# Optimization experiments

Measured on AMD Instinct MI355X. Metric: run time of the kernel, lower is better.

Reference implementation:

```python
import jax, jax.numpy as jnp
import numpy as np

N_ATOMS = 512
B = 14            # orbitals per atom (basis block size)
F = 128           # node feature dim
FE = 128          # edge feature dim
HID = 256
P = N_ATOMS * (N_ATOMS - 1) // 2


def setup_inputs() -> dict:
    key = jax.random.key(0)
    ks = jax.random.split(key, 12)
    s = 0.02  # small init scale for MLP weights
    pi, pj = jnp.triu_indices(N_ATOMS, k=1)
    return {
        "nodes_feature": jax.random.normal(ks[0], (N_ATOMS, F), jnp.float32),
        "edges_feature": jax.random.normal(ks[1], (N_ATOMS, N_ATOMS, FE), jnp.float32),
        "atom_blocks": jax.random.normal(ks[2], (N_ATOMS, B, B), jnp.float32),
        "overlap_pair": jax.random.normal(ks[3], (P, B, B), jnp.float32),
        "W1": jax.random.normal(ks[4], (F + FE, HID), jnp.float32) * s,
        "b1": jnp.zeros((HID,), jnp.float32),
        "W2": jax.random.normal(ks[5], (HID, B * B), jnp.float32) * s,
        "b2": jnp.zeros((B * B,), jnp.float32),
        "Wo1": jax.random.normal(ks[6], (2 * F + FE, HID), jnp.float32) * s,
        "bo1": jnp.zeros((HID,), jnp.float32),
        "Wo2": jax.random.normal(ks[7], (HID, B * B), jnp.float32) * s,
        "bo2": jnp.zeros((B * B,), jnp.float32),
        "pair_i": pi.astype(jnp.int32),
        "pair_j": pj.astype(jnp.int32),
    }


def reference(nodes_feature, edges_feature, atom_blocks, overlap_pair,
              W1, b1, W2, b2, Wo1, bo1, Wo2, bo2, pair_i, pair_j):
    n = nodes_feature.shape[0]
    ar = jnp.arange(n)

    # ---- diagonal blocks: MLP(node_i, edge_ii) -> BxB correction of atom block
    e_ii = edges_feature[ar, ar]                          # [N, FE]
    x = jnp.concatenate([nodes_feature, e_ii], axis=-1)   # [N, F+FE]
    h = jax.nn.silu(x @ W1 + b1)
    m = (h @ W2 + b2).reshape(n, B, B)
    diag_blocks = atom_blocks + m                         # [N, B, B]

    # ---- off-diagonal blocks: MLP(node_i, node_j, edge_ij) -> BxB correction
    ni = nodes_feature[pair_i]                            # [P, F]
    nj = nodes_feature[pair_j]                            # [P, F]
    eij = edges_feature[pair_i, pair_j]                   # [P, FE]
    xo = jnp.concatenate([ni, nj, eij], axis=-1)          # [P, 2F+FE]
    ho = jax.nn.silu(xo @ Wo1 + bo1)
    mo = (ho @ Wo2 + bo2).reshape(-1, B, B)
    off_blocks = overlap_pair + mo                        # [P, B, B]

    # ---- scatter blocks into dense Hamiltonian [N*B, N*B]
    Hm = jnp.zeros((n, B, n, B), dtype=nodes_feature.dtype)
    Hm = Hm.at[ar, :, ar, :].set(diag_blocks)
    Hm = Hm.at[pair_i, :, pair_j, :].set(off_blocks)
    Hm = Hm.at[pair_j, :, pair_i, :].set(jnp.transpose(off_blocks, (0, 2, 1)))
    return Hm.reshape(n * B, n * B)
```

## Files before the change

kernel.cpp:

```cpp
#include <hip/hip_runtime.h>
#include <stdint.h>

typedef unsigned short u16;
typedef unsigned int u32;
typedef __bf16 bf16x8 __attribute__((ext_vector_type(8)));
typedef float f32x4 __attribute__((ext_vector_type(4)));

#define N_ATOMS 512
#define BDIM 14
#define BB 196
#define FDIM 128
#define HROW 7168
#define NPAIR 130816
#define ROWS 64
#define NPBLK (NPAIR / ROWS)
#define NBLK  (NPBLK + N_ATOMS / ROWS)
#define HALFU (ROWS * BB / 2)

#define OFF_W1F   0
#define OFF_W2F   65536
#define OFF_WO1F  118784
#define OFF_WO2F  217088
#define WS_ELEMS  270336

__device__ __forceinline__ float b2f(u16 u) {
    union { u32 u; float f; } c; c.u = ((u32)u) << 16; return c.f;
}
__device__ __forceinline__ u16 fb(float f) {
    union { float f; u32 u; } c; c.f = f;
    u32 r = c.u + 0x7fff + ((c.u >> 16) & 1);
    return (u16)(r >> 16);
}
__device__ __forceinline__ bf16x8 ld16b(const u16* p) {
    return *(const bf16x8*)(const void*)p;
}
__device__ __forceinline__ bf16x8 ldcvt8(const float* p) {
    const float4 a = *(const float4*)(const void*)p;
    const float4 b = *(const float4*)(const void*)(p + 4);
    bf16x8 r;
    r[0] = (__bf16)a.x; r[1] = (__bf16)a.y; r[2] = (__bf16)a.z; r[3] = (__bf16)a.w;
    r[4] = (__bf16)b.x; r[5] = (__bf16)b.y; r[6] = (__bf16)b.z; r[7] = (__bf16)b.w;
    return r;
}

__global__ void prep_kernel(const float* __restrict__ W1, const float* __restrict__ W2,
                            const float* __restrict__ Wo1, const float* __restrict__ Wo2,
                            u16* __restrict__ ws) {
    int gid = blockIdx.x * 256 + threadIdx.x;
    const float* src; int idx, NT, Ncols, Nreal;
    if (gid < OFF_W2F)       { idx = gid;             src = W1;  NT = 16; Ncols = 256; Nreal = 256; }
    else if (gid < OFF_WO1F) { idx = gid - OFF_W2F;   src = W2;  NT = 13; Ncols = 196; Nreal = 196; }
    else if (gid < OFF_WO2F) { idx = gid - OFF_WO1F;  src = Wo1; NT = 16; Ncols = 256; Nreal = 256; }
    else                     { idx = gid - OFF_WO2F;  src = Wo2; NT = 13; Ncols = 196; Nreal = 196; }
    int jj   = idx & 7;
    int lane = (idx >> 3) & 63;
    int tile = idx >> 9;
    int nt = tile % NT;
    int ks = tile / NT;
    int k = ks * 32 + ((lane >> 4) << 3) + jj;
    int n = nt * 16 + (lane & 15);
    ws[gid] = (n < Nreal) ? fb(src[k * Ncols + n]) : (u16)0;
}

__global__ __launch_bounds__(256, 4)
void ham_main(const float* __restrict__ nodes, const float* __restrict__ edges,
              const float* __restrict__ atomb, const float* __restrict__ ovl,
              const float* __restrict__ b1v, const float* __restrict__ b2v,
              const float* __restrict__ bo1, const float* __restrict__ bo2,
              const int* __restrict__ pair_i, const int* __restrict__ pair_j,
              const u16* __restrict__ ws, float* __restrict__ out)
{
    __shared__ u16 sH[ROWS * 264];
    __shared__ int sI[ROWS], sJ[ROWS];
    const int tid = threadIdx.x;
    const int w = tid >> 6, lane = tid & 63;
    const int q = lane >> 4, l15 = lane & 15;
    const int bid = blockIdx.x;
    const bool isPair = bid < NPBLK;

    u32 offA[4], offB[4], offE[4];
    int KS1;
    const u16 *WAf, *WBf;
    const float *bias1, *bias2;
    const float *seg1base;

    if (isPair) {
        const int pbase = bid * ROWS;
        KS1 = 12; WAf = ws + OFF_WO1F; WBf = ws + OFF_WO2F; bias1 = bo1; bias2 = bo2;
        seg1base = nodes;
        if (tid < ROWS) { int p = pbase + tid; sI[tid] = pair_i[p]; sJ[tid] = pair_j[p]; }
        #pragma unroll
        for (int pp = 0; pp < 4; ++pp) {
            int p = pbase + pp * 16 + l15;
            int i = pair_i[p], j = pair_j[p];
            offA[pp] = (u32)i * FDIM;
            offB[pp] = (u32)j * FDIM;
            offE[pp] = ((u32)i * N_ATOMS + (u32)j) * FDIM;
        }
    } else {
        const int nbase = (bid - NPBLK) * ROWS;
        KS1 = 8; WAf = ws + OFF_W1F; WBf = ws + OFF_W2F; bias1 = b1v; bias2 = b2v;
        seg1base = edges;
        #pragma unroll
        for (int pp = 0; pp < 4; ++pp) {
            int nn = nbase + pp * 16 + l15;
            offA[pp] = (u32)nn * FDIM;
            offB[pp] = ((u32)nn * N_ATOMS + (u32)nn) * FDIM;
            offE[pp] = offB[pp];
        }
    }

    f32x4 acc[4][4];
    #pragma unroll
    for (int a = 0; a < 4; ++a)
        #pragma unroll
        for (int b = 0; b < 4; ++b)
            acc[a][b] = (f32x4){0.f, 0.f, 0.f, 0.f};

    for (int ks = 0; ks < KS1; ++ks) {
        const int seg = ks >> 2;
        const int koff = (ks & 3) * 32 + q * 8;
        const float* bse = (seg == 0) ? nodes : (seg == 1) ? seg1base : edges;
        bf16x8 bfr[4];
        #pragma unroll
        for (int pp = 0; pp < 4; ++pp) {
            const u32 off = (seg == 0) ? offA[pp] : (seg == 1) ? offB[pp] : offE[pp];
            bfr[pp] = ldcvt8(bse + off + koff);
        }
        const u16* ap = WAf + ((size_t)((ks * 16 + w * 4) * 64 + lane)) * 8;
        #pragma unroll
        for (int hh = 0; hh < 4; ++hh) {
            bf16x8 afr = ld16b(ap + (size_t)hh * 512);
            #pragma unroll
            for (int pp = 0; pp < 4; ++pp)
                acc[hh][pp] = __builtin_amdgcn_mfma_f32_16x16x32_bf16(afr, bfr[pp], acc[hh][pp], 0, 0, 0);
        }
    }

    #pragma unroll
    for (int hh = 0; hh < 4; ++hh) {
        const int h0 = w * 64 + hh * 16 + q * 4;
        const float bb0 = bias1[h0], bb1 = bias1[h0 + 1];
        const float bb2 = bias1[h0 + 2], bb3 = bias1[h0 + 3];
        #pragma unroll
        for (int pp = 0; pp < 4; ++pp) {
            const int row = pp * 16 + l15;
            float x0 = acc[hh][pp][0] + bb0, x1 = acc[hh][pp][1] + bb1;
            float x2 = acc[hh][pp][2] + bb2, x3 = acc[hh][pp][3] + bb3;
            float s0 = x0 / (1.f + __expf(-x0)), s1 = x1 / (1.f + __expf(-x1));
            float s2 = x2 / (1.f + __expf(-x2)), s3 = x3 / (1.f + __expf(-x3));
            uint2 pk;
            pk.x = (u32)fb(s0) | ((u32)fb(s1) << 16);
            pk.y = (u32)fb(s2) | ((u32)fb(s3) << 16);
            *(uint2*)(void*)&sH[row * 264 + h0] = pk;
        }
    }
    __syncthreads();

    f32x4 acc2[13];
    #pragma unroll
    for (int n = 0; n < 13; ++n)
        acc2[n] = (f32x4){0.f, 0.f, 0.f, 0.f};

    const int row2 = w * 16 + l15;
    for (int ks = 0; ks < 8; ++ks) {
        bf16x8 a2 = ld16b(&sH[row2 * 264 + ks * 32 + q * 8]);
        const u16* bp = WBf + ((size_t)((ks * 13) * 64 + lane)) * 8;
        #pragma unroll
        for (int nt = 0; nt < 13; ++nt) {
            bf16x8 bfr = ld16b(bp + (size_t)nt * 512);
            acc2[nt] = __builtin_amdgcn_mfma_f32_16x16x32_bf16(a2, bfr, acc2[nt], 0, 0, 0);
        }
    }
    __syncthreads();

    u16* sOut = sH;
    const float* addsrc = isPair ? (ovl + (size_t)bid * ROWS * BB)
                                 : (atomb + (size_t)(bid - NPBLK) * ROWS * BB);
    const int pr = w * 16 + q * 4;
    #pragma unroll
    for (int nt = 0; nt < 13; ++nt) {
        const int e = nt * 16 + l15;
        if (e < BB) {
            const float be = bias2[e];
            #pragma unroll
            for (int r = 0; r < 4; ++r) {
                float v = acc2[nt][r] + be + addsrc[(size_t)(pr + r) * BB + e];
                sOut[(pr + r) * BB + e] = fb(v);
            }
        }
    }
    __syncthreads();

    if (isPair) {
        for (int u = tid; u < HALFU; u += 256) {
            const int a = u / 448;
            const int r = u - a * 448;
            const int pl = r / 7;
            const int c2 = (r - pl * 7) * 2;
            const int i = sI[pl], j = sJ[pl];
            u32 v = *(const u32*)(const void*)(sOut + pl * BB + a * 14 + c2);
            float2 o; o.x = b2f((u16)v); o.y = b2f((u16)(v >> 16));
            size_t addr = (size_t)(i * 14 + a) * HROW + j * 14 + c2;
            *(float2*)(void*)(out + addr) = o;
        }
        for (int u = tid; u < HALFU; u += 256) {
            const int pl = u / 98;
            const int r = u - pl * 98;
            const int b = r / 7;
            const int a2i = (r - b * 7) * 2;
            const int i = sI[pl], j = sJ[pl];
            float2 o;
            o.x = b2f(sOut[pl * BB + a2i * 14 + b]);
            o.y = b2f(sOut[pl * BB + (a2i + 1) * 14 + b]);
            size_t addr = (size_t)(j * 14 + b) * HROW + i * 14 + a2i;
            *(float2*)(void*)(out + addr) = o;
        }
    } else {
        const int nbase = (bid - NPBLK) * ROWS;
        for (int u = tid; u < HALFU; u += 256) {
            const int a = u / 448;
            const int r = u - a * 448;
            const int pl = r / 7;
            const int c2 = (r - pl * 7) * 2;
            const int nn = nbase + pl;
            u32 v = *(const u32*)(const void*)(sOut + pl * BB + a * 14 + c2);
            float2 o; o.x = b2f((u16)v); o.y = b2f((u16)(v >> 16));
            size_t addr = (size_t)(nn * 14 + a) * HROW + nn * 14 + c2;
            *(float2*)(void*)(out + addr) = o;
        }
    }
}

extern "C" void kernel_launch(void* const* d_in, const int* in_sizes, int n_in,
                              void* d_out, int out_size, void* d_ws, size_t ws_size,
                              hipStream_t stream) {
    const float* nodes = (const float*)d_in[0];
    const float* edges = (const float*)d_in[1];
    const float* atomb = (const float*)d_in[2];
    const float* ovl   = (const float*)d_in[3];
    const float* W1    = (const float*)d_in[4];
    const float* b1    = (const float*)d_in[5];
    const float* W2    = (const float*)d_in[6];
    const float* b2    = (const float*)d_in[7];
    const float* Wo1   = (const float*)d_in[8];
    const float* bo1   = (const float*)d_in[9];
    const float* Wo2   = (const float*)d_in[10];
    const float* bo2   = (const float*)d_in[11];
    const int* pi      = (const int*)d_in[12];
    const int* pj      = (const int*)d_in[13];
    u16* ws    = (u16*)d_ws;
    float* out = (float*)d_out;

    prep_kernel<<<WS_ELEMS / 256, 256, 0, stream>>>(W1, W2, Wo1, Wo2, ws);
    ham_main<<<NBLK, 256, 0, stream>>>(nodes, edges, atomb, ovl,
                                       b1, b2, bo1, bo2, pi, pj, ws, out);
}
```

Before: 518.6 us.

## Stage gathered MLP inputs in LDS and rebalance second GEMM across waves

The first GEMM no longer has each wave gather and convert its own fp32 rows from global memory. The block now cooperatively loads each row's node and edge features with coalesced float4 reads, packs them to bf16 into a shared tile, and feeds the MFMAs from LDS. The second GEMM now splits the 13 output column tiles across the four waves, with each wave covering all 64 rows, so each weight fragment is reused four times instead of each wave reloading every tile. Shared memory grows to 392-element rows, and launch bounds drop from 4 to 3 blocks per SM, which trades occupancy for the extra LDS and registers.

```diff
diff --git a/kernel.cpp b/kernel.cpp
--- a/kernel.cpp
+++ b/kernel.cpp
@@ -7,7 +7,6 @@
 typedef float f32x4 __attribute__((ext_vector_type(4)));
 
 #define N_ATOMS 512
-#define BDIM 14
 #define BB 196
 #define FDIM 128
 #define HROW 7168
@@ -17,6 +16,9 @@
 #define NBLK  (NPBLK + N_ATOMS / ROWS)
 #define HALFU (ROWS * BB / 2)
 
+#define XS 392
+#define HS 264
+
 #define OFF_W1F   0
 #define OFF_W2F   65536
 #define OFF_WO1F  118784
@@ -34,13 +36,11 @@
 __device__ __forceinline__ bf16x8 ld16b(const u16* p) {
     return *(const bf16x8*)(const void*)p;
 }
-__device__ __forceinline__ bf16x8 ldcvt8(const float* p) {
-    const float4 a = *(const float4*)(const void*)p;
-    const float4 b = *(const float4*)(const void*)(p + 4);
-    bf16x8 r;
-    r[0] = (__bf16)a.x; r[1] = (__bf16)a.y; r[2] = (__bf16)a.z; r[3] = (__bf16)a.w;
-    r[4] = (__bf16)b.x; r[5] = (__bf16)b.y; r[6] = (__bf16)b.z; r[7] = (__bf16)b.w;
-    return r;
+__device__ __forceinline__ uint2 pk4(float4 v) {
+    union { __bf16 h[4]; uint2 u; } c;
+    c.h[0] = (__bf16)v.x; c.h[1] = (__bf16)v.y;
+    c.h[2] = (__bf16)v.z; c.h[3] = (__bf16)v.w;
+    return c.u;
 }
 
 __global__ void prep_kernel(const float* __restrict__ W1, const float* __restrict__ W2,
@@ -62,53 +62,31 @@
     ws[gid] = (n < Nreal) ? fb(src[k * Ncols + n]) : (u16)0;
 }
 
-__global__ __launch_bounds__(256, 4)
-void ham_main(const float* __restrict__ nodes, const float* __restrict__ edges,
-              const float* __restrict__ atomb, const float* __restrict__ ovl,
-              const float* __restrict__ b1v, const float* __restrict__ b2v,
-              const float* __restrict__ bo1, const float* __restrict__ bo2,
-              const int* __restrict__ pair_i, const int* __restrict__ pair_j,
-              const u16* __restrict__ ws, float* __restrict__ out)
+template<int KS1>
+__device__ __forceinline__ void mlp_tile(
+    const float* __restrict__ sb0, const float* __restrict__ sb1,
+    const float* __restrict__ sb2,
+    const u16* __restrict__ WAf, const u16* __restrict__ WBf,
+    const float* __restrict__ bias1, const float* __restrict__ bias2,
+    const float* __restrict__ addsrc,
+    u16* sX, const int tid)
 {
-    __shared__ u16 sH[ROWS * 264];
-    __shared__ int sI[ROWS], sJ[ROWS];
-    const int tid = threadIdx.x;
+    constexpr int NSEG = KS1 / 4;
     const int w = tid >> 6, lane = tid & 63;
     const int q = lane >> 4, l15 = lane & 15;
-    const int bid = blockIdx.x;
-    const bool isPair = bid < NPBLK;
-
-    u32 offA[4], offB[4], offE[4];
-    int KS1;
-    const u16 *WAf, *WBf;
-    const float *bias1, *bias2;
-    const float *seg1base;
-
-    if (isPair) {
-        const int pbase = bid * ROWS;
-        KS1 = 12; WAf = ws + OFF_WO1F; WBf = ws + OFF_WO2F; bias1 = bo1; bias2 = bo2;
-        seg1base = nodes;
-        if (tid < ROWS) { int p = pbase + tid; sI[tid] = pair_i[p]; sJ[tid] = pair_j[p]; }
-        #pragma unroll
-        for (int pp = 0; pp < 4; ++pp) {
-            int p = pbase + pp * 16 + l15;
-            int i = pair_i[p], j = pair_j[p];
-            offA[pp] = (u32)i * FDIM;
-            offB[pp] = (u32)j * FDIM;
-            offE[pp] = ((u32)i * N_ATOMS + (u32)j) * FDIM;
-        }
-    } else {
-        const int nbase = (bid - NPBLK) * ROWS;
-        KS1 = 8; WAf = ws + OFF_W1F; WBf = ws + OFF_W2F; bias1 = b1v; bias2 = b2v;
-        seg1base = edges;
-        #pragma unroll
-        for (int pp = 0; pp < 4; ++pp) {
-            int nn = nbase + pp * 16 + l15;
-            offA[pp] = (u32)nn * FDIM;
-            offB[pp] = ((u32)nn * N_ATOMS + (u32)nn) * FDIM;
-            offE[pp] = offB[pp];
-        }
-    }
+    const int srow = tid >> 2, ssub = tid & 3;
+
+    #pragma unroll
+    for (int seg = 0; seg < NSEG; ++seg) {
+        const float* rb = (seg == 0) ? sb0 : (seg == 1) ? sb1 : sb2;
+        #pragma unroll
+        for (int it = 0; it < 8; ++it) {
+            const int f0 = it * 16 + ssub * 4;
+            const float4 v = *(const float4*)(const void*)(rb + f0);
+            *(uint2*)(void*)&sX[srow * XS + seg * 128 + f0] = pk4(v);
+        }
+    }
+    __syncthreads();
 
     f32x4 acc[4][4];
     #pragma unroll
@@ -117,26 +95,26 @@
         for (int b = 0; b < 4; ++b)
             acc[a][b] = (f32x4){0.f, 0.f, 0.f, 0.f};
 
+    #pragma unroll
     for (int ks = 0; ks < KS1; ++ks) {
-        const int seg = ks >> 2;
-        const int koff = (ks & 3) * 32 + q * 8;
-        const float* bse = (seg == 0) ? nodes : (seg == 1) ? seg1base : edges;
+        const int xoff = ks * 32 + q * 8;
         bf16x8 bfr[4];
         #pragma unroll
-        for (int pp = 0; pp < 4; ++pp) {
-            const u32 off = (seg == 0) ? offA[pp] : (seg == 1) ? offB[pp] : offE[pp];
-            bfr[pp] = ldcvt8(bse + off + koff);
-        }
-        const u16* ap = WAf + ((size_t)((ks * 16 + w * 4) * 64 + lane)) * 8;
+        for (int pp = 0; pp < 4; ++pp)
+            bfr[pp] = ld16b(&sX[(pp * 16 + l15) * XS + xoff]);
+        const u16* ap = WAf + (size_t)((ks * 16 + w * 4) * 64 + lane) * 8;
         #pragma unroll
         for (int hh = 0; hh < 4; ++hh) {
             bf16x8 afr = ld16b(ap + (size_t)hh * 512);
-            #pragma unroll
-            for (int pp = 0; pp < 4; ++pp)
-                acc[hh][pp] = __builtin_amdgcn_mfma_f32_16x16x32_bf16(afr, bfr[pp], acc[hh][pp], 0, 0, 0);
-        }
-    }
-
+            acc[hh][0] = __builtin_amdgcn_mfma_f32_16x16x32_bf16(afr, bfr[0], acc[hh][0], 0, 0, 0);
+            acc[hh][1] = __builtin_amdgcn_mfma_f32_16x16x32_bf16(afr, bfr[1], acc[hh][1], 0, 0, 0);
+            acc[hh][2] = __builtin_amdgcn_mfma_f32_16x16x32_bf16(afr, bfr[2], acc[hh][2], 0, 0, 0);
+            acc[hh][3] = __builtin_amdgcn_mfma_f32_16x16x32_bf16(afr, bfr[3], acc[hh][3], 0, 0, 0);
+        }
+    }
+    __syncthreads();
+
+    u16* sH = sX;
     #pragma unroll
     for (int hh = 0; hh < 4; ++hh) {
         const int h0 = w * 64 + hh * 16 + q * 4;
@@ -152,56 +130,102 @@
             uint2 pk;
             pk.x = (u32)fb(s0) | ((u32)fb(s1) << 16);
             pk.y = (u32)fb(s2) | ((u32)fb(s3) << 16);
-            *(uint2*)(void*)&sH[row * 264 + h0] = pk;
-        }
-    }
-    __syncthreads();
-
-    f32x4 acc2[13];
-    #pragma unroll
-    for (int n = 0; n < 13; ++n)
-        acc2[n] = (f32x4){0.f, 0.f, 0.f, 0.f};
-
-    const int row2 = w * 16 + l15;
+            *(uint2*)(void*)&sH[row * HS + h0] = pk;
+        }
+    }
+    __syncthreads();
+
+    const int ntLo = (w == 0) ? 0 : 1 + 3 * w;
+    const int ntN  = (w == 0) ? 4 : 3;
+
+    f32x4 acc2[4][4];
+    #pragma unroll
+    for (int a = 0; a < 4; ++a)
+        #pragma unroll
+        for (int b = 0; b < 4; ++b)
+            acc2[a][b] = (f32x4){0.f, 0.f, 0.f, 0.f};
+
+    #pragma unroll
     for (int ks = 0; ks < 8; ++ks) {
-        bf16x8 a2 = ld16b(&sH[row2 * 264 + ks * 32 + q * 8]);
-        const u16* bp = WBf + ((size_t)((ks * 13) * 64 + lane)) * 8;
-        #pragma unroll
-        for (int nt = 0; nt < 13; ++nt) {
-            bf16x8 bfr = ld16b(bp + (size_t)nt * 512);
-            acc2[nt] = __builtin_amdgcn_mfma_f32_16x16x32_bf16(a2, bfr, acc2[nt], 0, 0, 0);
-        }
-    }
-    __syncthreads();
-
-    u16* sOut = sH;
-    const float* addsrc = isPair ? (ovl + (size_t)bid * ROWS * BB)
-                                 : (atomb + (size_t)(bid - NPBLK) * ROWS * BB);
-    const int pr = w * 16 + q * 4;
-    #pragma unroll
-    for (int nt = 0; nt < 13; ++nt) {
-        const int e = nt * 16 + l15;
-        if (e < BB) {
-            const float be = bias2[e];
-            #pragma unroll
-            for (int r = 0; r < 4; ++r) {
-                float v = acc2[nt][r] + be + addsrc[(size_t)(pr + r) * BB + e];
-                sOut[(pr + r) * BB + e] = fb(v);
+        bf16x8 a2[4];
+        #pragma unroll
+        for (int mm = 0; mm < 4; ++mm)
+            a2[mm] = ld16b(&sH[(mm * 16 + l15) * HS + ks * 32 + q * 8]);
+        #pragma unroll
+        for (int ntl = 0; ntl < 4; ++ntl) {
+            if (ntl < ntN) {
+                const int nt = ntLo + ntl;
+                bf16x8 bfr = ld16b(WBf + (size_t)((ks * 13 + nt) * 64 + lane) * 8);
+                #pragma unroll
+                for (int mm = 0; mm < 4; ++mm)
+                    acc2[mm][ntl] = __builtin_amdgcn_mfma_f32_16x16x32_bf16(a2[mm], bfr, acc2[mm][ntl], 0, 0, 0);
             }
         }
     }
     __syncthreads();
 
+    u16* sOut = sX;
+    #pragma unroll
+    for (int ntl = 0; ntl < 4; ++ntl) {
+        if (ntl < ntN) {
+            const int e = (ntLo + ntl) * 16 + l15;
+            if (e < BB) {
+                const float be = bias2[e];
+                #pragma unroll
+                for (int mm = 0; mm < 4; ++mm) {
+                    const int pr = mm * 16 + q * 4;
+                    #pragma unroll
+                    for (int r = 0; r < 4; ++r) {
+                        float v = acc2[mm][ntl][r] + be + addsrc[(size_t)(pr + r) * BB + e];
+                        sOut[(pr + r) * BB + e] = fb(v);
+                    }
+                }
+            }
+        }
+    }
+    __syncthreads();
+}
+
+__global__ __launch_bounds__(256, 3)
+void ham_main(const float* __restrict__ nodes, const float* __restrict__ edges,
+              const float* __restrict__ atomb, const float* __restrict__ ovl,
+              const float* __restrict__ b1v, const float* __restrict__ b2v,
+              const float* __restrict__ bo1, const float* __restrict__ bo2,
+              const int* __restrict__ pair_i, const int* __restrict__ pair_j,
+              const u16* __restrict__ ws, float* __restrict__ out)
+{
+    __shared__ u16 sX[ROWS * XS];
+    __shared__ int sI[ROWS], sJ[ROWS];
+    const int tid = threadIdx.x;
+    const int bid = blockIdx.x;
+    const bool isPair = bid < NPBLK;
+    const int srow = tid >> 2;
+
+    if (isPair && tid < ROWS) {
+        int p = bid * ROWS + tid;
+        sI[tid] = pair_i[p]; sJ[tid] = pair_j[p];
+    }
+    __syncthreads();
+
     if (isPair) {
+        const int pbase = bid * ROWS;
+        const int i = sI[srow], j = sJ[srow];
+        mlp_tile<12>(nodes + (size_t)i * FDIM,
+                     nodes + (size_t)j * FDIM,
+                     edges + ((size_t)i * N_ATOMS + (size_t)j) * FDIM,
+                     ws + OFF_WO1F, ws + OFF_WO2F, bo1, bo2,
+                     ovl + (size_t)pbase * BB, sX, tid);
+
+        u16* sOut = sX;
         for (int u = tid; u < HALFU; u += 256) {
             const int a = u / 448;
             const int r = u - a * 448;
             const int pl = r / 7;
             const int c2 = (r - pl * 7) * 2;
-            const int i = sI[pl], j = sJ[pl];
+            const int i2 = sI[pl], j2 = sJ[pl];
             u32 v = *(const u32*)(const void*)(sOut + pl * BB + a * 14 + c2);
             float2 o; o.x = b2f((u16)v); o.y = b2f((u16)(v >> 16));
-            size_t addr = (size_t)(i * 14 + a) * HROW + j * 14 + c2;
+            size_t addr = (size_t)(i2 * 14 + a) * HROW + j2 * 14 + c2;
             *(float2*)(void*)(out + addr) = o;
         }
         for (int u = tid; u < HALFU; u += 256) {
@@ -209,24 +233,31 @@
             const int r = u - pl * 98;
             const int b = r / 7;
             const int a2i = (r - b * 7) * 2;
-            const int i = sI[pl], j = sJ[pl];
+            const int i2 = sI[pl], j2 = sJ[pl];
             float2 o;
             o.x = b2f(sOut[pl * BB + a2i * 14 + b]);
             o.y = b2f(sOut[pl * BB + (a2i + 1) * 14 + b]);
-            size_t addr = (size_t)(j * 14 + b) * HROW + i * 14 + a2i;
+            size_t addr = (size_t)(j2 * 14 + b) * HROW + i2 * 14 + a2i;
             *(float2*)(void*)(out + addr) = o;
         }
     } else {
         const int nbase = (bid - NPBLK) * ROWS;
+        const int nn = nbase + srow;
+        const float* erow = edges + (size_t)nn * (N_ATOMS + 1) * FDIM;
+        mlp_tile<8>(nodes + (size_t)nn * FDIM, erow, erow,
+                    ws + OFF_W1F, ws + OFF_W2F, b1v, b2v,
+                    atomb + (size_t)nbase * BB, sX, tid);
+
+        u16* sOut = sX;
         for (int u = tid; u < HALFU; u += 256) {
             const int a = u / 448;
             const int r = u - a * 448;
             const int pl = r / 7;
             const int c2 = (r - pl * 7) * 2;
-            const int nn = nbase + pl;
+            const int n2 = nbase + pl;
             u32 v = *(const u32*)(const void*)(sOut + pl * BB + a * 14 + c2);
             float2 o; o.x = b2f((u16)v); o.y = b2f((u16)(v >> 16));
-            size_t addr = (size_t)(nn * 14 + a) * HROW + nn * 14 + c2;
+            size_t addr = (size_t)(n2 * 14 + a) * HROW + n2 * 14 + c2;
             *(float2*)(void*)(out + addr) = o;
         }
     }
```

Measured after the change: 504.2 us. 1.03x faster.
